# Performance work log

Measured on AMD Instinct MI355X. Metric: run time of the kernel, lower is better.

## Reference

```python
import jax, jax.numpy as jnp
import numpy as np

DIM = 512
QK_DIM = 128
HID = int(2.0 * DIM)  # expansion_factor * dim
OUT_DIM = 8
LN_EPS = 1e-5


def _layernorm(x, g, b):
    mu = jnp.mean(x, axis=-1, keepdims=True)
    var = jnp.var(x, axis=-1, keepdims=True)
    return (x - mu) * jax.lax.rsqrt(var + LN_EPS) * g + b


def setup_inputs() -> dict:
    key = jax.random.key(0)
    ks = jax.random.split(key, 8)
    x = jax.random.normal(ks[0], (4, 4096, DIM), dtype=jnp.float32)
    # parameters (torch Linear: y = x @ W.T + b; we store W already transposed)
    Wh = jax.random.normal(ks[1], (DIM, 2 * HID), dtype=jnp.float32) * (1.0 / np.sqrt(DIM))
    bh = jnp.zeros((2 * HID,), dtype=jnp.float32)
    Wqk = jax.random.normal(ks[2], (DIM, QK_DIM), dtype=jnp.float32) * (1.0 / np.sqrt(DIM))
    bqk = jnp.zeros((QK_DIM,), dtype=jnp.float32)
    gamma = jax.random.normal(ks[3], (2, QK_DIM), dtype=jnp.float32) * 0.02
    beta = jnp.zeros((2, QK_DIM), dtype=jnp.float32)
    Wo = jax.random.normal(ks[4], (HID, OUT_DIM), dtype=jnp.float32) * (1.0 / np.sqrt(HID))
    bo = jnp.zeros((OUT_DIM,), dtype=jnp.float32)
    ln_g = jnp.ones((DIM,), dtype=jnp.float32)
    ln_b = jnp.zeros((DIM,), dtype=jnp.float32)
    return {"x": x, "ln_g": ln_g, "ln_b": ln_b, "Wh": Wh, "bh": bh,
            "Wqk": Wqk, "bqk": bqk, "gamma": gamma, "beta": beta,
            "Wo": Wo, "bo": bo}


def reference(x, ln_g, ln_b, Wh, bh, Wqk, bqk, gamma, beta, Wo, bo):
    seq_len = x.shape[-2]
    normed = _layernorm(x, ln_g, ln_b)                       # [b,s,dim]
    hidden = jax.nn.silu(normed @ Wh + bh)                   # [b,s,2*hid]
    v, gate = jnp.split(hidden, 2, axis=-1)                  # each [b,s,hid]
    Z = jax.nn.silu(normed @ Wqk + bqk)                      # [b,s,qk]
    QK = Z[..., None, :] * gamma + beta                      # [b,s,2,qk]
    q = QK[..., 0, :]
    k = QK[..., 1, :]
    sim = jnp.einsum('bid,bjd->bij', q, k) / seq_len         # [b,s,s]
    A = jnp.square(jax.nn.relu(sim))                         # ReLU^2 attention
    V = jnp.einsum('bij,bjd->bid', A, v) * gate              # [b,s,hid]
    out = V @ Wo + bo                                        # [b,s,8]
    return out
```

## Files before the change

kernel.cpp:

```cpp
#include <hip/hip_runtime.h>
#include <stdint.h>

#define DIM   512
#define QKD   128
#define HID   1024
#define HID2  2048
#define OUTD  8
#define BATCH 4
#define SEQ   4096
#define ROWS  (BATCH*SEQ)
#define LN_EPS 1e-5f

typedef unsigned short u16;
typedef unsigned int   u32;
typedef __bf16 bf16x8 __attribute__((ext_vector_type(8)));
typedef float  f32x4  __attribute__((ext_vector_type(4)));

__device__ inline u16 f2bf(float f){
    uint32_t u = __builtin_bit_cast(uint32_t, f);
    u += 0x7FFFu + ((u >> 16) & 1u);
    return (u16)(u >> 16);
}
__device__ inline float bf2f(u16 h){
    uint32_t u = ((uint32_t)h) << 16;
    return __builtin_bit_cast(float, u);
}
__device__ inline void split_bf16(float x, u16 &hi, u16 &lo){
    hi = f2bf(x);
    float r = x - bf2f(hi);
    lo = f2bf(r);
}
__device__ inline bf16x8 ld_frag(const u16* p){
    uint4 r = *reinterpret_cast<const uint4*>(p);
    return __builtin_bit_cast(bf16x8, r);
}
__device__ inline f32x4 mfma16(bf16x8 a, bf16x8 b, f32x4 c){
    return __builtin_amdgcn_mfma_f32_16x16x32_bf16(a, b, c, 0, 0, 0);
}
__device__ inline float silu(float x){ return x / (1.f + expf(-x)); }
__device__ inline void gload_lds16(const u16* g, u16* l){
    __builtin_amdgcn_global_load_lds(
        (const __attribute__((address_space(1))) u32*)g,
        (__attribute__((address_space(3))) u32*)l, 16, 0, 0);
}

__global__ void prep_split(const float* __restrict__ Wh, const float* __restrict__ Wqk,
                           const float* __restrict__ Wo,
                           u16* whth, u16* wqkth, u16* wqktl, u16* woT){
    int tid = blockIdx.x*256 + threadIdx.x;
    const int NWH = HID2*DIM;
    if (tid < NWH){
        int k = tid & (DIM-1);
        int n = tid >> 9;
        whth[tid] = f2bf(Wh[(size_t)k*HID2 + n]);
    } else if (tid < NWH + QKD*DIM){
        int t2 = tid - NWH;
        int k = t2 & (DIM-1);
        int n = t2 >> 9;
        float w = Wqk[(size_t)k*QKD + n];
        u16 h,l; split_bf16(w,h,l);
        wqkth[t2]=h; wqktl[t2]=l;
    } else {
        int t3 = tid - NWH - QKD*DIM;
        if (t3 < 32*512){
            int dt = t3 >> 9, l = (t3 >> 3) & 63, e = t3 & 7;
            int o  = l & 15, dl = ((l >> 4) << 3) + e;
            woT[t3] = (o < OUTD) ? f2bf(Wo[(size_t)(dt*32 + dl)*OUTD + o]) : (u16)0;
        }
    }
}

__global__ __launch_bounds__(256) void ln_kernel(const float* __restrict__ x,
                                                 const float* __restrict__ g,
                                                 const float* __restrict__ b,
                                                 u16* nh){
    int wave = threadIdx.x >> 6, lane = threadIdx.x & 63;
    int row  = blockIdx.x*4 + wave;
    const float* xr = x + (size_t)row*DIM;
    float4 v0 = *(const float4*)(xr + lane*8);
    float4 v1 = *(const float4*)(xr + lane*8 + 4);
    float xs[8] = {v0.x,v0.y,v0.z,v0.w,v1.x,v1.y,v1.z,v1.w};
    float s = 0.f, q = 0.f;
    #pragma unroll
    for (int i=0;i<8;++i){ s += xs[i]; q += xs[i]*xs[i]; }
    #pragma unroll
    for (int m=1;m<64;m<<=1){ s += __shfl_xor(s,m,64); q += __shfl_xor(q,m,64); }
    float mean = s * (1.f/DIM);
    float var  = q * (1.f/DIM) - mean*mean;
    float rstd = rsqrtf(var + LN_EPS);
    float4 g0 = *(const float4*)(g + lane*8);
    float4 g1 = *(const float4*)(g + lane*8 + 4);
    float4 b0 = *(const float4*)(b + lane*8);
    float4 b1 = *(const float4*)(b + lane*8 + 4);
    float gs[8] = {g0.x,g0.y,g0.z,g0.w,g1.x,g1.y,g1.z,g1.w};
    float bs[8] = {b0.x,b0.y,b0.z,b0.w,b1.x,b1.y,b1.z,b1.w};
    u16 hh[8];
    #pragma unroll
    for (int i=0;i<8;++i){
        float nv = (xs[i]-mean)*rstd*gs[i] + bs[i];
        hh[i] = f2bf(nv);
    }
    size_t o = (size_t)row*DIM + lane*8;
    *(uint4*)(nh + o) = *(uint4*)hh;
}

__global__ __launch_bounds__(256,2) void gemm_h(
        const u16* __restrict__ nh,
        const u16* __restrict__ bth,
        const float* __restrict__ bh,
        u16* v_f, float* gate){
    __shared__ __align__(16) u16 SH2[16384];
    u16* SA = SH2;
    u16* SB = SH2 + 8192;
    const int bid = blockIdx.x;
    const int xcd = bid & 7, bx = bid >> 3;
    const int nb = xcd*2 + (bx >> 7);
    const int mb = bx & 127;
    const int n0 = nb*128, m0 = mb*128;
    const int w = threadIdx.x >> 6, lane = threadIdx.x & 63;
    const int wr = w >> 1, wc = w & 1;

    auto stage = [&](int ks, int p){
        #pragma unroll
        for (int c=0;c<2;++c){
            int row = w*32 + c*16 + (lane>>2);
            const u16* gA = nh  + (size_t)(m0+row)*DIM + ks*32 + (lane&3)*8;
            const u16* gB = bth + (size_t)(n0+row)*DIM + ks*32 + (lane&3)*8;
            int off = w*1024 + c*512;
            gload_lds16(gA, &SA[p*4096 + off]);
            gload_lds16(gB, &SB[p*4096 + off]);
        }
    };

    stage(0, 0);
    __syncthreads();

    f32x4 acc[4][4] = {};
    for (int ks=0; ks<16; ++ks){
        const int p = ks & 1;
        if (ks < 15) stage(ks+1, p^1);
        bf16x8 Ah[4];
        #pragma unroll
        for (int rf=0;rf<4;++rf)
            Ah[rf] = ld_frag(&SA[p*4096 + (wr*64 + rf*16 + (lane&15))*32 + (lane>>4)*8]);
        #pragma unroll
        for (int cf=0;cf<4;++cf){
            bf16x8 Bh = ld_frag(&SB[p*4096 + (wc*64 + cf*16 + (lane&15))*32 + (lane>>4)*8]);
            #pragma unroll
            for (int rf=0;rf<4;++rf)
                acc[rf][cf] = mfma16(Ah[rf], Bh, acc[rf][cf]);
        }
        __syncthreads();
    }
    if (nb < 8){
        u16* VP = SH2;
        #pragma unroll
        for (int rf=0;rf<4;++rf){
            #pragma unroll
            for (int cf=0;cf<4;++cf){
                #pragma unroll
                for (int r=0;r<4;++r){
                    int row_rel = wr*64 + rf*16 + (lane>>4)*4 + r;
                    int col_rel = wc*64 + cf*16 + (lane&15);
                    float s = silu(acc[rf][cf][r] + bh[n0 + col_rel]);
                    int f = ((row_rel>>5)<<3) | (col_rel>>4);
                    VP[f*512 + ((col_rel&15) + (((row_rel>>3)&3)<<4))*8 + (row_rel&7)] = f2bf(s);
                }
            }
        }
        __syncthreads();
        int fi = threadIdx.x >> 3, pt = threadIdx.x & 7;
        int b  = m0 >> 12, itb = (m0 & 4095) >> 5;
        size_t gbase = (((size_t)b*128 + itb + (fi>>3))*64 + (n0>>4) + (fi&7))*512;
        #pragma unroll
        for (int c2=0;c2<8;++c2)
            *(uint4*)(v_f + gbase + pt*64 + c2*8) = *(uint4*)&VP[fi*512 + pt*64 + c2*8];
    } else {
        #pragma unroll
        for (int rf=0;rf<4;++rf){
            #pragma unroll
            for (int cf=0;cf<4;++cf){
                #pragma unroll
                for (int r=0;r<4;++r){
                    int row = m0 + wr*64 + rf*16 + (lane>>4)*4 + r;
                    int col = n0 + wc*64 + cf*16 + (lane&15);
                    float s = silu(acc[rf][cf][r] + bh[col]);
                    gate[(size_t)row*HID + (col - HID)] = s;
                }
            }
        }
    }
}

__global__ __launch_bounds__(256,2) void gemm_qk(
        const u16* __restrict__ nh,
        const u16* __restrict__ bth, const u16* __restrict__ btl,
        const float* __restrict__ bqk, const float* __restrict__ gamma,
        const float* __restrict__ beta,
        u16* q_f, u16* k_f){
    __shared__ __align__(16) u16 At[64][40];
    __shared__ __align__(16) u16 Bt[2][128][40];
    int m0 = blockIdx.x * 64;
    int wave = threadIdx.x>>6, lane = threadIdx.x&63;
    int wr = wave>>1, wc = wave&1;
    f32x4 acc[2][4] = {};
    for (int ks=0; ks<16; ++ks){
        {
            int row = threadIdx.x>>2, ch = threadIdx.x&3;
            *(uint4*)&At[row][ch*8] = *(const uint4*)(nh + (size_t)(m0+row)*DIM + ks*32 + ch*8);
        }
        #pragma unroll
        for (int r=0;r<2;++r){
            int idx = r*256 + threadIdx.x;
            int row = idx>>2, ch = idx&3;
            size_t gb = (size_t)row*DIM + ks*32 + ch*8;
            *(uint4*)&Bt[0][row][ch*8] = *(const uint4*)(bth + gb);
            *(uint4*)&Bt[1][row][ch*8] = *(const uint4*)(btl + gb);
        }
        __syncthreads();
        bf16x8 Ah[2];
        #pragma unroll
        for (int rf=0;rf<2;++rf)
            Ah[rf] = ld_frag(&At[wr*32 + rf*16 + (lane&15)][(lane>>4)*8]);
        #pragma unroll
        for (int cf=0;cf<4;++cf){
            bf16x8 Bh = ld_frag(&Bt[0][wc*64 + cf*16 + (lane&15)][(lane>>4)*8]);
            bf16x8 Bl = ld_frag(&Bt[1][wc*64 + cf*16 + (lane&15)][(lane>>4)*8]);
            #pragma unroll
            for (int rf=0;rf<2;++rf){
                acc[rf][cf] = mfma16(Ah[rf], Bh, acc[rf][cf]);
                acc[rf][cf] = mfma16(Ah[rf], Bl, acc[rf][cf]);
            }
        }
        __syncthreads();
    }
    #pragma unroll
    for (int rf=0;rf<2;++rf){
        #pragma unroll
        for (int cf=0;cf<4;++cf){
            #pragma unroll
            for (int r=0;r<4;++r){
                int row = m0 + wr*32 + rf*16 + (lane>>4)*4 + r;
                int col = wc*64 + cf*16 + (lane&15);
                float z = silu(acc[rf][cf][r] + bqk[col]);
                float qv = z*gamma[col]       + beta[col];
                float kv = z*gamma[QKD + col] + beta[QKD + col];
                size_t lane_e = (size_t)((row&15) + (((col>>3)&3)<<4))*8 + (col&7);
                size_t it4ks  = (size_t)(row>>4)*4 + (col>>5);
                q_f[it4ks*512 + lane_e] = f2bf(qv);
                k_f[it4ks*512 + lane_e] = f2bf(kv);
            }
        }
    }
}

__global__ __launch_bounds__(512,4) void attn(
        const u16* __restrict__ q_f, const u16* __restrict__ k_f,
        const u16* __restrict__ v_f, const float* __restrict__ gate,
        const u16* __restrict__ woT, float* part){
    __shared__ __align__(16) u16 SH[33792];
    u16* QL = SH;
    u16* KT0 = SH + 8192;
    u16* AT0 = SH + 24576;
    const int bid = blockIdx.x, xcd = bid & 7;
    const int batch = xcd >> 1, dhalf = xcd & 1, qt = bid >> 3;
    const int i0 = qt * 64;
    const int w = threadIdx.x >> 6, lane = threadIdx.x & 63;
    const int fr = w >> 1, fc = w & 1;
    const int ds = w;

    {
        size_t qbase = ((size_t)(batch*256 + qt*4))*2048;
        size_t kbase = ((size_t)(batch*256 + 0*4))*2048;
        #pragma unroll
        for (int c=0;c<2;++c){
            int off = w*1024 + c*512;
            gload_lds16(q_f + qbase + off + lane*8, &QL[off]);
            gload_lds16(k_f + kbase + off + lane*8, &KT0[off]);
        }
    }
    __syncthreads();

    f32x4 acc[4][4] = {};
    for (int kt=0; kt<64; ++kt){
        const int p = kt & 1;
        {
            size_t kbase = ((size_t)(batch*256 + (((kt+1)&63))*4))*2048;
            #pragma unroll
            for (int c=0;c<2;++c){
                int off = w*1024 + c*512;
                gload_lds16(k_f + kbase + off + lane*8, &KT0[(p^1)*8192 + off]);
            }
        }
        bf16x8 vb0[4];
        #pragma unroll
        for (int dc=0;dc<4;++dc)
            vb0[dc] = ld_frag(v_f + (((size_t)(batch*128 + kt*2))*64
                              + dhalf*32 + ds*4 + dc)*512 + lane*8);
        f32x4 sacc[2] = {};
        #pragma unroll
        for (int ks=0;ks<4;++ks){
            bf16x8 qa = ld_frag(&QL[fr*2048 + ks*512 + lane*8]);
            #pragma unroll
            for (int t=0;t<2;++t){
                bf16x8 kb = ld_frag(&KT0[p*8192 + (fc*2 + t)*2048 + ks*512 + lane*8]);
                sacc[t] = mfma16(qa, kb, sacc[t]);
            }
        }
        u16* Ab = AT0 + p*4608;
        #pragma unroll
        for (int t=0;t<2;++t){
            #pragma unroll
            for (int r=0;r<4;++r){
                float s = sacc[t][r];
                s = s > 0.f ? s*s : 0.f;
                int q = fr*16 + (lane>>4)*4 + r;
                int j = fc*32 + t*16 + (lane&15);
                Ab[q*72 + j] = f2bf(s);
            }
        }
        __syncthreads();
        #pragma unroll
        for (int qr=0;qr<4;++qr){
            bf16x8 af = ld_frag(&Ab[(qr*16 + (lane&15))*72 + (lane>>4)*8]);
            #pragma unroll
            for (int dc=0;dc<4;++dc)
                acc[qr][dc] = mfma16(af, vb0[dc], acc[qr][dc]);
        }
        bf16x8 vb1[4];
        #pragma unroll
        for (int dc=0;dc<4;++dc)
            vb1[dc] = ld_frag(v_f + (((size_t)(batch*128 + kt*2 + 1))*64
                              + dhalf*32 + ds*4 + dc)*512 + lane*8);
        #pragma unroll
        for (int qr=0;qr<4;++qr){
            bf16x8 af = ld_frag(&Ab[(qr*16 + (lane&15))*72 + 32 + (lane>>4)*8]);
            #pragma unroll
            for (int dc=0;dc<4;++dc)
                acc[qr][dc] = mfma16(af, vb1[dc], acc[qr][dc]);
        }
    }
    __syncthreads();
    u16* VgL = SH;
    #pragma unroll
    for (int qr=0; qr<4; ++qr){
        #pragma unroll
        for (int dc=0; dc<4; ++dc){
            #pragma unroll
            for (int r=0; r<4; ++r){
                int i_local = qr*16 + (lane>>4)*4 + r;
                int d_local = ds*64 + dc*16 + (lane&15);
                float g = gate[((size_t)(batch*SEQ + i0 + i_local))*HID + dhalf*512 + d_local];
                float vg = acc[qr][dc][r] * g * 0x1p-24f;
                int dchunk = (d_local >> 5);
                int dl = d_local & 31;
                int q16 = (lane>>4)*4 + r;
                VgL[(dchunk*4 + qr)*512 + (q16 + ((dl>>3)<<4))*8 + (dl&7)] = f2bf(vg);
            }
        }
    }
    __syncthreads();
    if (w < 4){
        f32x4 oc = {};
        #pragma unroll
        for (int ch=0; ch<16; ++ch){
            bf16x8 a = ld_frag(&VgL[(ch*4 + w)*512 + lane*8]);
            bf16x8 b = ld_frag(woT + ((size_t)(dhalf*16 + ch))*512 + lane*8);
            oc = mfma16(a, b, oc);
        }
        if ((lane & 15) < OUTD){
            size_t base = ((size_t)dhalf*ROWS + batch*SEQ + i0 + w*16)*OUTD;
            #pragma unroll
            for (int r=0;r<4;++r)
                part[base + (size_t)((lane>>4)*4 + r)*OUTD + (lane&15)] = oc[r];
        }
    }
}

__global__ __launch_bounds__(256) void reduce_out(const float* __restrict__ part,
                                                  const float* __restrict__ bo,
                                                  float* __restrict__ out){
    int idx = (blockIdx.x*256 + threadIdx.x)*4;
    float4 a = *(const float4*)(part + idx);
    float4 b = *(const float4*)(part + (size_t)ROWS*OUTD + idx);
    float4 c = *(const float4*)(bo + (idx & 7));
    float4 o = {a.x+b.x+c.x, a.y+b.y+c.y, a.z+b.z+c.z, a.w+b.w+c.w};
    *(float4*)(out + idx) = o;
}

extern "C" void kernel_launch(void* const* d_in, const int* in_sizes, int n_in,
                              void* d_out, int out_size, void* d_ws, size_t ws_size,
                              hipStream_t stream){
    const float* x    = (const float*)d_in[0];
    const float* ln_g = (const float*)d_in[1];
    const float* ln_b = (const float*)d_in[2];
    const float* Wh   = (const float*)d_in[3];
    const float* bh   = (const float*)d_in[4];
    const float* Wqk  = (const float*)d_in[5];
    const float* bqk  = (const float*)d_in[6];
    const float* gamma= (const float*)d_in[7];
    const float* beta = (const float*)d_in[8];
    const float* Wo   = (const float*)d_in[9];
    const float* bo   = (const float*)d_in[10];
    float* out = (float*)d_out;

    char* w = (char*)d_ws;
    auto alloc = [&](size_t bytes)->char*{
        char* p = w; w += (bytes + 255) & ~(size_t)255; return p;
    };
    u16* nh    = (u16*)alloc((size_t)ROWS*DIM*2);
    u16* whth  = (u16*)alloc((size_t)HID2*DIM*2);
    u16* wqkth = (u16*)alloc((size_t)QKD*DIM*2);
    u16* wqktl = (u16*)alloc((size_t)QKD*DIM*2);
    u16* woT   = (u16*)alloc((size_t)32*512*2);
    u16* q_f   = (u16*)alloc((size_t)ROWS*QKD*2);
    u16* k_f   = (u16*)alloc((size_t)ROWS*QKD*2);
    u16* v_f   = (u16*)alloc((size_t)BATCH*HID*SEQ*2);
    float* gate= (float*)alloc((size_t)ROWS*HID*4);
    float* part= (float*)alloc((size_t)2*ROWS*OUTD*4);

    prep_split<<<(HID2*DIM + QKD*DIM + 32*512)/256, 256, 0, stream>>>(Wh, Wqk, Wo, whth, wqkth, wqktl, woT);
    ln_kernel<<<ROWS/4, 256, 0, stream>>>(x, ln_g, ln_b, nh);
    gemm_h<<<2048, 256, 0, stream>>>(nh, whth, bh, v_f, gate);
    gemm_qk<<<ROWS/64, 256, 0, stream>>>(nh, wqkth, wqktl, bqk, gamma, beta, q_f, k_f);
    attn<<<512, 512, 0, stream>>>(q_f, k_f, v_f, gate, woT, part);
    reduce_out<<<ROWS*OUTD/1024, 256, 0, stream>>>(part, bo, out);
}
```

Baseline: 273.1 us.

## Store gate as bf16 in MFMA fragment layout; double-buffer gemm_qk loads

The gate half of the hidden projection is now written as bf16 in a fragment-ordered layout, so each lane does one 8-byte store in gemm_h and one 8-byte load in attn instead of strided fp32 scalar accesses. This halves gate memory traffic and makes the accesses coalesced, at the cost of rounding gate to bf16. Separately, gemm_qk now uses direct global-to-LDS async loads with a two-stage double buffer, overlapping the next k-slice load with the current MFMAs.

After: 266.7 us. 1.02x faster.

```diff
diff --git a/kernel.cpp b/kernel.cpp
--- a/kernel.cpp
+++ b/kernel.cpp
@@ -108,7 +108,7 @@
         const u16* __restrict__ nh,
         const u16* __restrict__ bth,
         const float* __restrict__ bh,
-        u16* v_f, float* gate){
+        u16* v_f, u16* gate_f){
     __shared__ __align__(16) u16 SH2[16384];
     u16* SA = SH2;
     u16* SB = SH2 + 8192;
@@ -176,17 +176,22 @@
         for (int c2=0;c2<8;++c2)
             *(uint4*)(v_f + gbase + pt*64 + c2*8) = *(uint4*)&VP[fi*512 + pt*64 + c2*8];
     } else {
+        const int b  = m0 >> 12;
+        const int i_rel = m0 & 4095;
         #pragma unroll
         for (int rf=0;rf<4;++rf){
+            const int it = (i_rel + wr*64 + rf*16) >> 4;
             #pragma unroll
             for (int cf=0;cf<4;++cf){
+                const int dt = ((nb-8)*128 + wc*64 + cf*16) >> 4;
+                u16 gv[4];
                 #pragma unroll
                 for (int r=0;r<4;++r){
-                    int row = m0 + wr*64 + rf*16 + (lane>>4)*4 + r;
                     int col = n0 + wc*64 + cf*16 + (lane&15);
-                    float s = silu(acc[rf][cf][r] + bh[col]);
-                    gate[(size_t)row*HID + (col - HID)] = s;
+                    gv[r] = f2bf(silu(acc[rf][cf][r] + bh[col]));
                 }
+                size_t fo = (((size_t)b*256 + it)*64 + dt)*256 + lane*4;
+                *(uint2*)(gate_f + fo) = *(uint2*)gv;
             }
         }
     }
@@ -198,34 +203,42 @@
         const float* __restrict__ bqk, const float* __restrict__ gamma,
         const float* __restrict__ beta,
         u16* q_f, u16* k_f){
-    __shared__ __align__(16) u16 At[64][40];
-    __shared__ __align__(16) u16 Bt[2][128][40];
+    __shared__ __align__(16) u16 SA [2][2048];
+    __shared__ __align__(16) u16 SB0[2][4096];
+    __shared__ __align__(16) u16 SB1[2][4096];
     int m0 = blockIdx.x * 64;
-    int wave = threadIdx.x>>6, lane = threadIdx.x&63;
-    int wr = wave>>1, wc = wave&1;
+    int w = threadIdx.x >> 6, lane = threadIdx.x & 63;
+    int wr = w >> 1, wc = w & 1;
+
+    auto stage = [&](int ks, int p){
+        {
+            int row = w*16 + (lane>>2);
+            gload_lds16(nh + (size_t)(m0+row)*DIM + ks*32 + (lane&3)*8, &SA[p][w*512]);
+        }
+        #pragma unroll
+        for (int c=0;c<2;++c){
+            int row = w*32 + c*16 + (lane>>2);
+            int off = w*1024 + c*512;
+            gload_lds16(bth + (size_t)row*DIM + ks*32 + (lane&3)*8, &SB0[p][off]);
+            gload_lds16(btl + (size_t)row*DIM + ks*32 + (lane&3)*8, &SB1[p][off]);
+        }
+    };
+
+    stage(0, 0);
+    __syncthreads();
+
     f32x4 acc[2][4] = {};
     for (int ks=0; ks<16; ++ks){
-        {
-            int row = threadIdx.x>>2, ch = threadIdx.x&3;
-            *(uint4*)&At[row][ch*8] = *(const uint4*)(nh + (size_t)(m0+row)*DIM + ks*32 + ch*8);
-        }
-        #pragma unroll
-        for (int r=0;r<2;++r){
-            int idx = r*256 + threadIdx.x;
-            int row = idx>>2, ch = idx&3;
-            size_t gb = (size_t)row*DIM + ks*32 + ch*8;
-            *(uint4*)&Bt[0][row][ch*8] = *(const uint4*)(bth + gb);
-            *(uint4*)&Bt[1][row][ch*8] = *(const uint4*)(btl + gb);
-        }
-        __syncthreads();
+        const int p = ks & 1;
+        if (ks < 15) stage(ks+1, p^1);
         bf16x8 Ah[2];
         #pragma unroll
         for (int rf=0;rf<2;++rf)
-            Ah[rf] = ld_frag(&At[wr*32 + rf*16 + (lane&15)][(lane>>4)*8]);
+            Ah[rf] = ld_frag(&SA[p][(wr*32 + rf*16 + (lane&15))*32 + (lane>>4)*8]);
         #pragma unroll
         for (int cf=0;cf<4;++cf){
-            bf16x8 Bh = ld_frag(&Bt[0][wc*64 + cf*16 + (lane&15)][(lane>>4)*8]);
-            bf16x8 Bl = ld_frag(&Bt[1][wc*64 + cf*16 + (lane&15)][(lane>>4)*8]);
+            bf16x8 Bh = ld_frag(&SB0[p][(wc*64 + cf*16 + (lane&15))*32 + (lane>>4)*8]);
+            bf16x8 Bl = ld_frag(&SB1[p][(wc*64 + cf*16 + (lane&15))*32 + (lane>>4)*8]);
             #pragma unroll
             for (int rf=0;rf<2;++rf){
                 acc[rf][cf] = mfma16(Ah[rf], Bh, acc[rf][cf]);
@@ -256,7 +269,7 @@
 
 __global__ __launch_bounds__(512,4) void attn(
         const u16* __restrict__ q_f, const u16* __restrict__ k_f,
-        const u16* __restrict__ v_f, const float* __restrict__ gate,
+        const u16* __restrict__ v_f, const u16* __restrict__ gate_f,
         const u16* __restrict__ woT, float* part){
     __shared__ __align__(16) u16 SH[33792];
     u16* QL = SH;
@@ -346,12 +359,13 @@
     for (int qr=0; qr<4; ++qr){
         #pragma unroll
         for (int dc=0; dc<4; ++dc){
+            size_t fo = (((size_t)batch*256 + qt*4 + qr)*64 + dhalf*32 + ds*4 + dc)*256 + lane*4;
+            uint2 gvp = *(const uint2*)(gate_f + fo);
+            u16* gv = (u16*)&gvp;
             #pragma unroll
             for (int r=0; r<4; ++r){
-                int i_local = qr*16 + (lane>>4)*4 + r;
                 int d_local = ds*64 + dc*16 + (lane&15);
-                float g = gate[((size_t)(batch*SEQ + i0 + i_local))*HID + dhalf*512 + d_local];
-                float vg = acc[qr][dc][r] * g * 0x1p-24f;
+                float vg = acc[qr][dc][r] * bf2f(gv[r]) * 0x1p-24f;
                 int dchunk = (d_local >> 5);
                 int dl = d_local & 31;
                 int q16 = (lane>>4)*4 + r;
@@ -416,13 +430,13 @@
     u16* q_f   = (u16*)alloc((size_t)ROWS*QKD*2);
     u16* k_f   = (u16*)alloc((size_t)ROWS*QKD*2);
     u16* v_f   = (u16*)alloc((size_t)BATCH*HID*SEQ*2);
-    float* gate= (float*)alloc((size_t)ROWS*HID*4);
+    u16* gate_f= (u16*)alloc((size_t)ROWS*HID*2);
     float* part= (float*)alloc((size_t)2*ROWS*OUTD*4);
 
     prep_split<<<(HID2*DIM + QKD*DIM + 32*512)/256, 256, 0, stream>>>(Wh, Wqk, Wo, whth, wqkth, wqktl, woT);
     ln_kernel<<<ROWS/4, 256, 0, stream>>>(x, ln_g, ln_b, nh);
-    gemm_h<<<2048, 256, 0, stream>>>(nh, whth, bh, v_f, gate);
+    gemm_h<<<2048, 256, 0, stream>>>(nh, whth, bh, v_f, gate_f);
     gemm_qk<<<ROWS/64, 256, 0, stream>>>(nh, wqkth, wqktl, bqk, gamma, beta, q_f, k_f);
-    attn<<<512, 512, 0, stream>>>(q_f, k_f, v_f, gate, woT, part);
+    attn<<<512, 512, 0, stream>>>(q_f, k_f, v_f, gate_f, woT, part);
     reduce_out<<<ROWS*OUTD/1024, 256, 0, stream>>>(part, bo, out);
 }
```
